# Kernel optimization log

Measured on AMD Instinct MI355X. Metric: run time of the kernel, lower is better.

Reference implementation:

```python
import jax, jax.numpy as jnp
import numpy as np

N, E, G = 200000, 1200000, 2048
NODE_DIM, H = 5, 64
NEG_SLOPE = 0.2


def setup_inputs() -> dict:
    key = jax.random.key(0)
    ks = jax.random.split(key, 20)
    def glorot(k, shape):
        fan = sum(shape) if len(shape) > 1 else shape[0] + 1
        return jax.random.normal(k, shape, jnp.float32) * jnp.sqrt(2.0 / fan)
    inp = {
        'x': jax.random.normal(ks[0], (N, NODE_DIM), jnp.float32),
        'edge_index': jax.random.randint(ks[1], (2, E), 0, N, jnp.int64),
        'batch': jnp.sort(jax.random.randint(ks[2], (N,), 0, G, jnp.int64)),
        'embed_W': glorot(ks[3], (NODE_DIM, H)), 'embed_b': jnp.zeros((H,), jnp.float32),
        'g1_W': glorot(ks[4], (H, H)), 'g1_asrc': glorot(ks[5], (H,)), 'g1_adst': glorot(ks[6], (H,)), 'g1_b': jnp.zeros((H,), jnp.float32),
        'g2_W': glorot(ks[7], (H, H)), 'g2_asrc': glorot(ks[8], (H,)), 'g2_adst': glorot(ks[9], (H,)), 'g2_b': jnp.zeros((H,), jnp.float32),
        'fc1_W': glorot(ks[10], (2 * H, 64)), 'fc1_b': jnp.zeros((64,), jnp.float32),
        'fc2_W': glorot(ks[11], (64, 32)), 'fc2_b': jnp.zeros((32,), jnp.float32),
        'fc3_W': glorot(ks[12], (32, 1)), 'fc3_b': jnp.zeros((1,), jnp.float32),
    }
    return inp


def gat_conv(x, src, dst, W, a_src, a_dst, b):
    # x: [N, H] -> h: [N, H]; edges (with self-loops) src->dst
    h = x @ W
    alpha_s = h @ a_src  # [N]
    alpha_d = h @ a_dst  # [N]
    e = jax.nn.leaky_relu(alpha_s[src] + alpha_d[dst], NEG_SLOPE)  # [E']
    m = jax.ops.segment_max(e, dst, num_segments=N)
    w = jnp.exp(e - m[dst])
    denom = jax.ops.segment_sum(w, dst, num_segments=N)
    alpha = w / (denom[dst] + 1e-16)
    out = jax.ops.segment_sum(h[src] * alpha[:, None], dst, num_segments=N)
    return out + b


def reference(x, edge_index, batch, embed_W, embed_b,
              g1_W, g1_asrc, g1_adst, g1_b,
              g2_W, g2_asrc, g2_adst, g2_b,
              fc1_W, fc1_b, fc2_W, fc2_b, fc3_W, fc3_b):
    # add self loops once (PyG GATConv default add_self_loops=True)
    loops = jnp.arange(N, dtype=edge_index.dtype)
    src = jnp.concatenate([edge_index[0], loops])
    dst = jnp.concatenate([edge_index[1], loops])

    h = x @ embed_W + embed_b
    h = gat_conv(h, src, dst, g1_W, g1_asrc, g1_adst, g1_b)
    h = jax.nn.relu(h)
    h = gat_conv(h, src, dst, g2_W, g2_asrc, g2_adst, g2_b)

    # global mean / max pooling per graph
    cnt = jax.ops.segment_sum(jnp.ones((N,), h.dtype), batch, num_segments=G)
    mean = jax.ops.segment_sum(h, batch, num_segments=G) / jnp.maximum(cnt, 1.0)[:, None]
    mx = jax.ops.segment_max(h, batch, num_segments=G)
    mx = jnp.where(cnt[:, None] > 0, mx, 0.0)
    g = jnp.concatenate([mean, mx], axis=1)  # [G, 2H]

    g = jax.nn.relu(g @ fc1_W + fc1_b)
    g = jax.nn.relu(g @ fc2_W + fc2_b)
    return g @ fc3_W + fc3_b  # [G, 1]
```

## Files before the change

### kernel.cpp

```cpp
#include <hip/hip_runtime.h>
#include <hip/hip_bf16.h>
#include <hip/hip_fp16.h>

#define HD 64
#define NODE_DIM 5
#define NEG_SLOPE 0.2f
#define GT 64
#define BSH 9
#define BNODES 512
#define NBMAX 512
#define BCAP 4096
#define EPB 8
#define LDH 72

typedef _Float16 f16x8 __attribute__((ext_vector_type(8)));
typedef float f32x4 __attribute__((ext_vector_type(4)));

template <bool EMBED>
__global__ __launch_bounds__(256) void gemm_alpha_k(
    const void* __restrict__ hin, const float* __restrict__ embW,
    const float* __restrict__ embB, const float* __restrict__ W,
    const float* __restrict__ asrc, const float* __restrict__ adst,
    __half* __restrict__ hout, float* __restrict__ alpha_s,
    float* __restrict__ alpha_d, int* __restrict__ bcnt0, int N) {
    __shared__ _Float16 hs[GT * LDH];
    __shared__ _Float16 Wt[HD * LDH];
    __shared__ float xe[GT * NODE_DIM];
    __shared__ float we[NODE_DIM * HD + HD];
    const int t = threadIdx.x;
    const int n0 = blockIdx.x * GT;
    if (EMBED && blockIdx.x == 0) {
        for (int j = t; j < NBMAX; j += 256) bcnt0[j] = 0;
    }
    if (n0 >= N) return;
    const int rem = N - n0;

#pragma unroll
    for (int j = 0; j < 16; j++) {
        int idx = t + 256 * j;
        int k = idx >> 6, n = idx & 63;
        Wt[n * LDH + k] = (_Float16)W[idx];
    }

    if (EMBED) {
        const float* xin = (const float*)hin;
        for (int j = t; j < GT * NODE_DIM; j += 256)
            xe[j] = (j < rem * NODE_DIM) ? xin[(size_t)n0 * NODE_DIM + j] : 0.0f;
        for (int j = t; j < NODE_DIM * HD + HD; j += 256)
            we[j] = (j < NODE_DIM * HD) ? embW[j] : embB[j - NODE_DIM * HD];
        __syncthreads();
        int r = t >> 2, d0 = (t & 3) * 16;
#pragma unroll
        for (int jj = 0; jj < 16; jj++) {
            int d = d0 + jj;
            float acc = we[NODE_DIM * HD + d];
#pragma unroll
            for (int k = 0; k < NODE_DIM; k++)
                acc = fmaf(xe[r * NODE_DIM + k], we[k * HD + d], acc);
            hs[r * LDH + d] = (r < rem) ? (_Float16)acc : (_Float16)0.0f;
        }
    } else {
        const short4* g4 = (const short4*)((const __half*)hin + (size_t)n0 * HD);
#pragma unroll
        for (int j = 0; j < 4; j++) {
            int idx = t + 256 * j;
            int row = idx >> 4, c4 = idx & 15;
            short4 v = {0, 0, 0, 0};
            if (row < rem) v = g4[idx];
            *(short4*)(hs + row * LDH + c4 * 4) = v;
        }
    }
    __syncthreads();

    const int lane = t & 63;
    const int w = t >> 6;
    const int r16 = lane & 15;
    const int g = lane >> 4;

    const _Float16* hrow = hs + (w * 16 + r16) * LDH + g * 8;
    f16x8 b0 = *(const f16x8*)(hrow);
    f16x8 b1 = *(const f16x8*)(hrow + 32);

    f32x4 acc[4];
#pragma unroll
    for (int mt = 0; mt < 4; mt++) acc[mt] = (f32x4){0.f, 0.f, 0.f, 0.f};

#pragma unroll
    for (int mt = 0; mt < 4; mt++) {
        const _Float16* arow = Wt + (mt * 16 + r16) * LDH + g * 8;
        f16x8 a0 = *(const f16x8*)(arow);
        f16x8 a1 = *(const f16x8*)(arow + 32);
        acc[mt] = __builtin_amdgcn_mfma_f32_16x16x32_f16(a0, b0, acc[mt], 0, 0, 0);
        acc[mt] = __builtin_amdgcn_mfma_f32_16x16x32_f16(a1, b1, acc[mt], 0, 0, 0);
    }

    const int node = n0 + w * 16 + r16;
    float ps = 0.0f, pd = 0.0f;
    if (node < N) {
#pragma unroll
        for (int mt = 0; mt < 4; mt++) {
            float4 av = ((const float4*)asrc)[mt * 4 + g];
            float4 bv = ((const float4*)adst)[mt * 4 + g];
            ps += acc[mt][0] * av.x + acc[mt][1] * av.y +
                  acc[mt][2] * av.z + acc[mt][3] * av.w;
            pd += acc[mt][0] * bv.x + acc[mt][1] * bv.y +
                  acc[mt][2] * bv.z + acc[mt][3] * bv.w;
            short4 s;
            s.x = __half_as_short(__float2half_rn(acc[mt][0]));
            s.y = __half_as_short(__float2half_rn(acc[mt][1]));
            s.z = __half_as_short(__float2half_rn(acc[mt][2]));
            s.w = __half_as_short(__float2half_rn(acc[mt][3]));
            ((short4*)hout)[(size_t)node * 16 + mt * 4 + g] = s;
        }
    }
    ps += __shfl_xor(ps, 16);
    ps += __shfl_xor(ps, 32);
    pd += __shfl_xor(pd, 16);
    pd += __shfl_xor(pd, 32);
    if (g == 0 && node < N) {
        alpha_s[node] = ps;
        alpha_d[node] = pd;
    }
}


__global__ __launch_bounds__(256) void partition_k(
    const int* __restrict__ ei, int* __restrict__ bcnt,
    int* __restrict__ bpack, int E) {
    __shared__ int lcnt[NBMAX], lbase[NBMAX];
    int dst[EPB], src[EPB];
    int jb = blockIdx.x * (256 * EPB) + threadIdx.x;
#pragma unroll
    for (int u = 0; u < EPB; u++) {
        int j = jb + u * 256;
        if (j < E) {
            dst[u] = __builtin_nontemporal_load(&ei[E + j]);
            src[u] = __builtin_nontemporal_load(&ei[j]);
        } else dst[u] = -1;
    }
    for (int b = threadIdx.x; b < NBMAX; b += 256) lcnt[b] = 0;
    __syncthreads();
#pragma unroll
    for (int u = 0; u < EPB; u++)
        if (dst[u] >= 0) atomicAdd(&lcnt[dst[u] >> BSH], 1);
    __syncthreads();
    for (int b = threadIdx.x; b < NBMAX; b += 256) {
        int c = lcnt[b];
        lbase[b] = c ? (b * BCAP + atomicAdd(&bcnt[b], c)) : 0;
        lcnt[b] = 0;
    }
    __syncthreads();
#pragma unroll
    for (int u = 0; u < EPB; u++) {
        if (dst[u] >= 0) {
            int b = dst[u] >> BSH;
            int o = atomicAdd(&lcnt[b], 1);
            bpack[lbase[b] + o] = (src[u] << BSH) | (dst[u] & (BNODES - 1));
        }
    }
}

__global__ __launch_bounds__(256) void bucket_csr_k(
    const int* __restrict__ bpack, const int* __restrict__ bcnt,
    int* __restrict__ off, int* __restrict__ csr_src, int N, int NB) {
    __shared__ int s[BNODES];
    __shared__ int lcur[BNODES];
    __shared__ int sred[256];
    const int t = threadIdx.x;
    const int b = blockIdx.x;
    const int nbase = b << BSH;
    const int cnt = bcnt[b];
    const int w0 = b * BCAP;

    int part = 0;
    for (int j = t; j < b; j += 256) part += bcnt[j];
    sred[t] = part;
    s[t] = 0; s[t + 256] = 0;
    __syncthreads();
#pragma unroll
    for (int o = 128; o; o >>= 1) {
        if (t < o) sred[t] += sred[t + o];
        __syncthreads();
    }
    const int e0 = sred[0];

    for (int j = t; j < cnt; j += 256)
        atomicAdd(&s[bpack[w0 + j] & (BNODES - 1)], 1);
    __syncthreads();
    int d0 = s[t], d1 = s[t + 256];
#pragma unroll
    for (int o = 1; o < BNODES; o <<= 1) {
        int a0 = (t >= o) ? s[t - o] : 0;
        int a1 = (t + 256 >= o) ? s[t + 256 - o] : 0;
        __syncthreads();
        s[t] += a0;
        s[t + 256] += a1;
        __syncthreads();
    }
    int ex0 = s[t] - d0, ex1 = s[t + 256] - d1;
    lcur[t] = ex0; lcur[t + 256] = ex1;
    int n0 = nbase + t, n1 = nbase + t + 256;
    if (n0 < N) off[n0] = e0 + ex0;
    if (n1 < N) off[n1] = e0 + ex1;
    if (t == 0 && b == NB - 1) off[N] = e0 + cnt;
    __syncthreads();
    for (int j = t; j < cnt; j += 256) {
        int v = bpack[w0 + j];
        int pos = atomicAdd(&lcur[v & (BNODES - 1)], 1);
        csr_src[e0 + pos] = v >> BSH;
    }
}

template <bool BR>
__global__ __launch_bounds__(256) void gather_k(
    const int* __restrict__ off, const int* __restrict__ csr_src,
    const float* __restrict__ as, const float* __restrict__ ad,
    const __half* __restrict__ h, const float* __restrict__ bias,
    __half* __restrict__ out, int N) {
    int tid = blockIdx.x * blockDim.x + threadIdx.x;
    int wv = tid >> 6;
    int lane = threadIdx.x & 63;
    int grp = lane >> 4;
    int l16 = lane & 15;
    int n = wv * 4 + grp;
    if (n >= N) return;
    int s0 = off[n], s1 = off[n + 1];
    float adv = ad[n];
    const short4* h4 = (const short4*)h;

    float e = as[n] + adv;
    e = (e >= 0.0f) ? e : NEG_SLOPE * e;
    float wsl = __expf(e);
    float l0 = wsl, l1 = 0.0f;
    short4 hvs = h4[(unsigned)(n * 16 + l16)];
    float4 acc0, acc1 = {0, 0, 0, 0};
    acc0.x = wsl * __half2float(__short_as_half(hvs.x));
    acc0.y = wsl * __half2float(__short_as_half(hvs.y));
    acc0.z = wsl * __half2float(__short_as_half(hvs.z));
    acc0.w = wsl * __half2float(__short_as_half(hvs.w));

    const int last = s1 - 1;
    for (int i = s0; i < s1; i += 8) {
        int src[8];
        short4 hv[8];
        float wt[8];
#pragma unroll
        for (int u = 0; u < 8; u++) {
            int idx = i + u;
            src[u] = csr_src[idx < s1 ? idx : last];
        }
#pragma unroll
        for (int u = 0; u < 8; u++)
            hv[u] = h4[(unsigned)(src[u] * 16 + l16)];
#pragma unroll
        for (int u = 0; u < 8; u++) {
            float e0 = as[src[u]] + adv;
            e0 = (e0 >= 0.0f) ? e0 : NEG_SLOPE * e0;
            float w0 = __expf(e0);
            wt[u] = (i + u < s1) ? w0 : 0.0f;
        }
#pragma unroll
        for (int u = 0; u < 8; u += 2) {
            l0 += wt[u];
            l1 += wt[u + 1];
            acc0.x = fmaf(wt[u], __half2float(__short_as_half(hv[u].x)), acc0.x);
            acc0.y = fmaf(wt[u], __half2float(__short_as_half(hv[u].y)), acc0.y);
            acc0.z = fmaf(wt[u], __half2float(__short_as_half(hv[u].z)), acc0.z);
            acc0.w = fmaf(wt[u], __half2float(__short_as_half(hv[u].w)), acc0.w);
            acc1.x = fmaf(wt[u + 1], __half2float(__short_as_half(hv[u + 1].x)), acc1.x);
            acc1.y = fmaf(wt[u + 1], __half2float(__short_as_half(hv[u + 1].y)), acc1.y);
            acc1.z = fmaf(wt[u + 1], __half2float(__short_as_half(hv[u + 1].z)), acc1.z);
            acc1.w = fmaf(wt[u + 1], __half2float(__short_as_half(hv[u + 1].w)), acc1.w);
        }
    }
    float inv = 1.0f / (l0 + l1 + 1e-16f);
    float4 r;
    r.x = (acc0.x + acc1.x) * inv;
    r.y = (acc0.y + acc1.y) * inv;
    r.z = (acc0.z + acc1.z) * inv;
    r.w = (acc0.w + acc1.w) * inv;
    if (BR) {
        float4 b = ((const float4*)bias)[l16];
        r.x = fmaxf(r.x + b.x, 0.0f);
        r.y = fmaxf(r.y + b.y, 0.0f);
        r.z = fmaxf(r.z + b.z, 0.0f);
        r.w = fmaxf(r.w + b.w, 0.0f);
    }
    short4 o;
    o.x = __half_as_short(__float2half_rn(r.x));
    o.y = __half_as_short(__float2half_rn(r.y));
    o.z = __half_as_short(__float2half_rn(r.z));
    o.w = __half_as_short(__float2half_rn(r.w));
    ((short4*)out)[(unsigned)(n * 16 + l16)] = o;
}

__global__ __launch_bounds__(256) void pool_mlp_k(
    const __half* __restrict__ hfin, const float* __restrict__ hb,
    const int* __restrict__ batch, int N,
    const float* __restrict__ fc1W, const float* __restrict__ fc1b,
    const float* __restrict__ fc2W, const float* __restrict__ fc2b,
    const float* __restrict__ fc3W, const float* __restrict__ fc3b,
    float* __restrict__ out) {
    __shared__ float psum[16][64];
    __shared__ float pmax[16][64];
    __shared__ float lds[192];
    int g = blockIdx.x;
    int t = threadIdx.x;
    int gg = t >> 4;
    int l16 = t & 15;
    int lo = 0, hi = N;
    while (lo < hi) { int mid = (lo + hi) >> 1; if (batch[mid] < g) lo = mid + 1; else hi = mid; }
    int start = lo;
    lo = start; hi = N;
    while (lo < hi) { int mid = (lo + hi) >> 1; if (batch[mid] < g + 1) lo = mid + 1; else hi = mid; }
    int end = lo;
    const short4* h4 = (const short4*)hfin;
    float4 sum = {0, 0, 0, 0};
    float4 mx = {-INFINITY, -INFINITY, -INFINITY, -INFINITY};
    for (int n = start + gg; n < end; n += 16) {
        short4 v = h4[(size_t)n * 16 + l16];
        float a = __half2float(__short_as_half(v.x));
        float b = __half2float(__short_as_half(v.y));
        float c = __half2float(__short_as_half(v.z));
        float d = __half2float(__short_as_half(v.w));
        sum.x += a; sum.y += b; sum.z += c; sum.w += d;
        mx.x = fmaxf(mx.x, a); mx.y = fmaxf(mx.y, b);
        mx.z = fmaxf(mx.z, c); mx.w = fmaxf(mx.w, d);
    }
    *(float4*)&psum[gg][l16 * 4] = sum;
    *(float4*)&pmax[gg][l16 * 4] = mx;
    __syncthreads();
    if (t < 64) {
        float s = 0.0f, m = -INFINITY;
#pragma unroll
        for (int k = 0; k < 16; k++) {
            s += psum[k][t];
            m = fmaxf(m, pmax[k][t]);
        }
        int cnt = end - start;
        float bias = hb[t];
        lds[t]      = (cnt > 0) ? s / (float)cnt + bias : 0.0f;
        lds[64 + t] = (cnt > 0) ? m + bias : 0.0f;
    }
    __syncthreads();
    if (t < 64) {
        int lane = t;
        float o1 = fc1b[lane];
        for (int k = 0; k < 128; k++) o1 += lds[k] * fc1W[k * 64 + lane];
        o1 = fmaxf(o1, 0.0f);
        __builtin_amdgcn_s_barrier();
        lds[128 + lane] = o1;
        float o2 = 0.0f;
        if (lane < 32) {
            o2 = fc2b[lane];
            for (int k = 0; k < 64; k++) o2 += lds[128 + k] * fc2W[k * 32 + lane];
            o2 = fmaxf(o2, 0.0f);
        }
        float part = (lane < 32) ? o2 * fc3W[lane] : 0.0f;
#pragma unroll
        for (int off = 32; off; off >>= 1) part += __shfl_xor(part, off);
        if (lane == 0) out[g] = part + fc3b[0];
    }
}

static inline size_t align256(size_t x) { return (x + 255) & ~(size_t)255; }

extern "C" void kernel_launch(void* const* d_in, const int* in_sizes, int n_in,
                              void* d_out, int out_size, void* d_ws, size_t ws_size,
                              hipStream_t stream) {
    const float* x      = (const float*)d_in[0];
    const int*   ei     = (const int*)d_in[1];
    const int*   batch  = (const int*)d_in[2];
    const float* embW   = (const float*)d_in[3];
    const float* embB   = (const float*)d_in[4];
    const float* g1W    = (const float*)d_in[5];
    const float* g1as   = (const float*)d_in[6];
    const float* g1ad   = (const float*)d_in[7];
    const float* g1b    = (const float*)d_in[8];
    const float* g2W    = (const float*)d_in[9];
    const float* g2as   = (const float*)d_in[10];
    const float* g2ad   = (const float*)d_in[11];
    const float* g2b    = (const float*)d_in[12];
    const float* fc1W   = (const float*)d_in[13];
    const float* fc1b   = (const float*)d_in[14];
    const float* fc2W   = (const float*)d_in[15];
    const float* fc2b   = (const float*)d_in[16];
    const float* fc3W   = (const float*)d_in[17];
    const float* fc3b   = (const float*)d_in[18];
    float* out = (float*)d_out;

    const int N  = in_sizes[0] / NODE_DIM;
    const int E  = in_sizes[1] / 2;
    const int G  = out_size;
    const int NH = N * HD;
    const int NB = (N + BNODES - 1) >> BSH;

    char* ws = (char*)d_ws;
    __half* bufA    = (__half*)ws; ws += align256((size_t)NH * 2);
    __half* bufB    = (__half*)ws; ws += align256((size_t)NH * 2);
    float*  as_buf  = (float*)ws;  ws += align256((size_t)N * 4);
    float*  ad_buf  = (float*)ws;  ws += align256((size_t)N * 4);
    int*    off     = (int*)ws;    ws += align256((size_t)(N + 1) * 4);
    int*    bcnt    = (int*)ws;    ws += align256((size_t)NBMAX * 4);
    int*    bpack   = (int*)ws;    ws += align256((size_t)NB * BCAP * 4);
    int*    csrsrc  = (int*)ws;    ws += align256((size_t)E * 4);

    const int B = 256;
    dim3 blk(B);
    dim3 gr_gemm((N + GT - 1) / GT);
    dim3 gr_gath(((N + 3) / 4 * 64 + B - 1) / B);
    dim3 gr_epb((E + B * EPB - 1) / (B * EPB));

    gemm_alpha_k<true><<<gr_gemm, blk, 0, stream>>>(x, embW, embB, g1W, g1as, g1ad,
                                                    bufB, as_buf, ad_buf, bcnt, N);
    partition_k<<<gr_epb, blk, 0, stream>>>(ei, bcnt, bpack, E);
    bucket_csr_k<<<dim3(NB), blk, 0, stream>>>(bpack, bcnt, off, csrsrc, N, NB);

    gather_k<true><<<gr_gath, blk, 0, stream>>>(off, csrsrc, as_buf, ad_buf,
                                                bufB, g1b, bufA, N);

    gemm_alpha_k<false><<<gr_gemm, blk, 0, stream>>>(bufA, nullptr, nullptr, g2W,
                                                     g2as, g2ad, bufB, as_buf, ad_buf,
                                                     nullptr, N);
    gather_k<false><<<gr_gath, blk, 0, stream>>>(off, csrsrc, as_buf, ad_buf,
                                                 bufB, nullptr, bufA, N);

    pool_mlp_k<<<dim3(G), dim3(256), 0, stream>>>(bufA, g2b, batch, N,
                                                  fc1W, fc1b, fc2W, fc2b, fc3W, fc3b, out);
}
```

Baseline: 262.5 us.

## Fuse embedding GEMM and edge partition into one interleaved launch, sort partition writes

Merges the layer-1 embed+GEMM kernel and the edge partition kernel into a single launch whose blocks are interleaved by role, so the two independent stages can run concurrently on the GPU. The partition blocks now sort edges in shared memory by bucket with a prefix scan before writing, so the bpack stores go out in contiguous runs instead of scattered. The bucket counters are zeroed by a separate tiny kernel, which adds one launch. It also adds a shared-memory scan with many barriers and a per-element binary search.

```diff
diff --git a/kernel.cpp b/kernel.cpp
--- a/kernel.cpp
+++ b/kernel.cpp
@@ -16,22 +16,108 @@
 typedef _Float16 f16x8 __attribute__((ext_vector_type(8)));
 typedef float f32x4 __attribute__((ext_vector_type(4)));
 
-template <bool EMBED>
-__global__ __launch_bounds__(256) void gemm_alpha_k(
-    const void* __restrict__ hin, const float* __restrict__ embW,
+
+__global__ void zero_k(int* __restrict__ p, int total) {
+    int i = blockIdx.x * blockDim.x + threadIdx.x;
+    if (i < total) p[i] = 0;
+}
+
+union FusedSM {
+    struct {
+        _Float16 hs[GT * LDH];
+        _Float16 Wt[HD * LDH];
+        float xe[GT * NODE_DIM];
+        float we[NODE_DIM * HD + HD];
+    } g;
+    struct {
+        int lcnt[NBMAX];
+        int lbase[NBMAX];
+        int lexc[NBMAX];
+        int cur[NBMAX];
+        int sorted[256 * EPB];
+    } p;
+};
+
+__global__ __launch_bounds__(256) void fused_embed_part_k(
+    const float* __restrict__ xin, const float* __restrict__ embW,
     const float* __restrict__ embB, const float* __restrict__ W,
     const float* __restrict__ asrc, const float* __restrict__ adst,
     __half* __restrict__ hout, float* __restrict__ alpha_s,
-    float* __restrict__ alpha_d, int* __restrict__ bcnt0, int N) {
-    __shared__ _Float16 hs[GT * LDH];
-    __shared__ _Float16 Wt[HD * LDH];
-    __shared__ float xe[GT * NODE_DIM];
-    __shared__ float we[NODE_DIM * HD + HD];
+    float* __restrict__ alpha_d, int N,
+    const int* __restrict__ ei, int* __restrict__ bcnt,
+    int* __restrict__ bpack, int E, int PB, int TOT) {
+    __shared__ FusedSM sm;
     const int t = threadIdx.x;
-    const int n0 = blockIdx.x * GT;
-    if (EMBED && blockIdx.x == 0) {
-        for (int j = t; j < NBMAX; j += 256) bcnt0[j] = 0;
-    }
+    const int bid = blockIdx.x;
+    const int p_before = (int)(((long long)bid * PB) / TOT);
+    const int p_after  = (int)(((long long)(bid + 1) * PB) / TOT);
+    const bool is_part = p_after > p_before;
+
+    if (is_part) {
+        const int pbid = p_before;
+        int dst[EPB], src[EPB];
+        int jb = pbid * (256 * EPB) + t;
+#pragma unroll
+        for (int u = 0; u < EPB; u++) {
+            int j = jb + u * 256;
+            if (j < E) {
+                dst[u] = __builtin_nontemporal_load(&ei[E + j]);
+                src[u] = __builtin_nontemporal_load(&ei[j]);
+            } else dst[u] = -1;
+        }
+        sm.p.lcnt[t] = 0; sm.p.lcnt[t + 256] = 0;
+        __syncthreads();
+#pragma unroll
+        for (int u = 0; u < EPB; u++)
+            if (dst[u] >= 0) atomicAdd(&sm.p.lcnt[dst[u] >> BSH], 1);
+        __syncthreads();
+        sm.p.lexc[t] = sm.p.lcnt[t];
+        sm.p.lexc[t + 256] = sm.p.lcnt[t + 256];
+        __syncthreads();
+        int c0 = sm.p.lexc[t], c1 = sm.p.lexc[t + 256];
+#pragma unroll
+        for (int o = 1; o < NBMAX; o <<= 1) {
+            int a0 = (t >= o) ? sm.p.lexc[t - o] : 0;
+            int a1 = (t + 256 >= o) ? sm.p.lexc[t + 256 - o] : 0;
+            __syncthreads();
+            sm.p.lexc[t] += a0;
+            sm.p.lexc[t + 256] += a1;
+            __syncthreads();
+        }
+        int e0 = sm.p.lexc[t] - c0, e1 = sm.p.lexc[t + 256] - c1;
+        __syncthreads();
+        sm.p.lexc[t] = e0; sm.p.lexc[t + 256] = e1;
+        sm.p.cur[t] = e0;  sm.p.cur[t + 256] = e1;
+        {
+            int c = sm.p.lcnt[t];
+            sm.p.lbase[t] = c ? t * BCAP + atomicAdd(&bcnt[t], c) : 0;
+            c = sm.p.lcnt[t + 256];
+            sm.p.lbase[t + 256] = c ? (t + 256) * BCAP + atomicAdd(&bcnt[t + 256], c) : 0;
+        }
+        __syncthreads();
+#pragma unroll
+        for (int u = 0; u < EPB; u++) {
+            if (dst[u] >= 0) {
+                int b = dst[u] >> BSH;
+                int pp = atomicAdd(&sm.p.cur[b], 1);
+                sm.p.sorted[pp] = (src[u] << BSH) | (dst[u] & (BNODES - 1));
+            }
+        }
+        __syncthreads();
+        const int tot = sm.p.lexc[NBMAX - 1] + sm.p.lcnt[NBMAX - 1];
+        for (int j = t; j < tot; j += 256) {
+            int lo = 0, hi = NBMAX - 1;
+            while (lo < hi) {
+                int mid = (lo + hi + 1) >> 1;
+                if (sm.p.lexc[mid] <= j) lo = mid; else hi = mid - 1;
+            }
+            bpack[sm.p.lbase[lo] + (j - sm.p.lexc[lo])] = sm.p.sorted[j];
+        }
+        return;
+    }
+
+    const int gidx = bid - p_before;
+    const int n0 = gidx * GT;
     if (n0 >= N) return;
     const int rem = N - n0;
 
@@ -39,35 +125,23 @@
     for (int j = 0; j < 16; j++) {
         int idx = t + 256 * j;
         int k = idx >> 6, n = idx & 63;
-        Wt[n * LDH + k] = (_Float16)W[idx];
-    }
-
-    if (EMBED) {
-        const float* xin = (const float*)hin;
-        for (int j = t; j < GT * NODE_DIM; j += 256)
-            xe[j] = (j < rem * NODE_DIM) ? xin[(size_t)n0 * NODE_DIM + j] : 0.0f;
-        for (int j = t; j < NODE_DIM * HD + HD; j += 256)
-            we[j] = (j < NODE_DIM * HD) ? embW[j] : embB[j - NODE_DIM * HD];
-        __syncthreads();
+        sm.g.Wt[n * LDH + k] = (_Float16)W[idx];
+    }
+    for (int j = t; j < GT * NODE_DIM; j += 256)
+        sm.g.xe[j] = (j < rem * NODE_DIM) ? xin[(size_t)n0 * NODE_DIM + j] : 0.0f;
+    for (int j = t; j < NODE_DIM * HD + HD; j += 256)
+        sm.g.we[j] = (j < NODE_DIM * HD) ? embW[j] : embB[j - NODE_DIM * HD];
+    __syncthreads();
+    {
         int r = t >> 2, d0 = (t & 3) * 16;
 #pragma unroll
         for (int jj = 0; jj < 16; jj++) {
             int d = d0 + jj;
-            float acc = we[NODE_DIM * HD + d];
+            float acc = sm.g.we[NODE_DIM * HD + d];
 #pragma unroll
             for (int k = 0; k < NODE_DIM; k++)
-                acc = fmaf(xe[r * NODE_DIM + k], we[k * HD + d], acc);
-            hs[r * LDH + d] = (r < rem) ? (_Float16)acc : (_Float16)0.0f;
-        }
-    } else {
-        const short4* g4 = (const short4*)((const __half*)hin + (size_t)n0 * HD);
-#pragma unroll
-        for (int j = 0; j < 4; j++) {
-            int idx = t + 256 * j;
-            int row = idx >> 4, c4 = idx & 15;
-            short4 v = {0, 0, 0, 0};
-            if (row < rem) v = g4[idx];
-            *(short4*)(hs + row * LDH + c4 * 4) = v;
+                acc = fmaf(sm.g.xe[r * NODE_DIM + k], sm.g.we[k * HD + d], acc);
+            sm.g.hs[r * LDH + d] = (r < rem) ? (_Float16)acc : (_Float16)0.0f;
         }
     }
     __syncthreads();
@@ -77,17 +151,16 @@
     const int r16 = lane & 15;
     const int g = lane >> 4;
 
-    const _Float16* hrow = hs + (w * 16 + r16) * LDH + g * 8;
+    const _Float16* hrow = sm.g.hs + (w * 16 + r16) * LDH + g * 8;
     f16x8 b0 = *(const f16x8*)(hrow);
     f16x8 b1 = *(const f16x8*)(hrow + 32);
 
     f32x4 acc[4];
 #pragma unroll
     for (int mt = 0; mt < 4; mt++) acc[mt] = (f32x4){0.f, 0.f, 0.f, 0.f};
-
 #pragma unroll
     for (int mt = 0; mt < 4; mt++) {
-        const _Float16* arow = Wt + (mt * 16 + r16) * LDH + g * 8;
+        const _Float16* arow = sm.g.Wt + (mt * 16 + r16) * LDH + g * 8;
         f16x8 a0 = *(const f16x8*)(arow);
         f16x8 a1 = *(const f16x8*)(arow + 32);
         acc[mt] = __builtin_amdgcn_mfma_f32_16x16x32_f16(a0, b0, acc[mt], 0, 0, 0);
@@ -123,40 +196,84 @@
     }
 }
 
-
-__global__ __launch_bounds__(256) void partition_k(
-    const int* __restrict__ ei, int* __restrict__ bcnt,
-    int* __restrict__ bpack, int E) {
-    __shared__ int lcnt[NBMAX], lbase[NBMAX];
-    int dst[EPB], src[EPB];
-    int jb = blockIdx.x * (256 * EPB) + threadIdx.x;
-#pragma unroll
-    for (int u = 0; u < EPB; u++) {
-        int j = jb + u * 256;
-        if (j < E) {
-            dst[u] = __builtin_nontemporal_load(&ei[E + j]);
-            src[u] = __builtin_nontemporal_load(&ei[j]);
-        } else dst[u] = -1;
-    }
-    for (int b = threadIdx.x; b < NBMAX; b += 256) lcnt[b] = 0;
-    __syncthreads();
-#pragma unroll
-    for (int u = 0; u < EPB; u++)
-        if (dst[u] >= 0) atomicAdd(&lcnt[dst[u] >> BSH], 1);
-    __syncthreads();
-    for (int b = threadIdx.x; b < NBMAX; b += 256) {
-        int c = lcnt[b];
-        lbase[b] = c ? (b * BCAP + atomicAdd(&bcnt[b], c)) : 0;
-        lcnt[b] = 0;
-    }
-    __syncthreads();
-#pragma unroll
-    for (int u = 0; u < EPB; u++) {
-        if (dst[u] >= 0) {
-            int b = dst[u] >> BSH;
-            int o = atomicAdd(&lcnt[b], 1);
-            bpack[lbase[b] + o] = (src[u] << BSH) | (dst[u] & (BNODES - 1));
-        }
+__global__ __launch_bounds__(256) void gemm_alpha_k(
+    const __half* __restrict__ hin, const float* __restrict__ W,
+    const float* __restrict__ asrc, const float* __restrict__ adst,
+    __half* __restrict__ hout, float* __restrict__ alpha_s,
+    float* __restrict__ alpha_d, int N) {
+    __shared__ _Float16 hs[GT * LDH];
+    __shared__ _Float16 Wt[HD * LDH];
+    const int t = threadIdx.x;
+    const int n0 = blockIdx.x * GT;
+    if (n0 >= N) return;
+    const int rem = N - n0;
+
+#pragma unroll
+    for (int j = 0; j < 16; j++) {
+        int idx = t + 256 * j;
+        int k = idx >> 6, n = idx & 63;
+        Wt[n * LDH + k] = (_Float16)W[idx];
+    }
+    {
+        const short4* g4 = (const short4*)(hin + (size_t)n0 * HD);
+#pragma unroll
+        for (int j = 0; j < 4; j++) {
+            int idx = t + 256 * j;
+            int row = idx >> 4, c4 = idx & 15;
+            short4 v = {0, 0, 0, 0};
+            if (row < rem) v = g4[idx];
+            *(short4*)(hs + row * LDH + c4 * 4) = v;
+        }
+    }
+    __syncthreads();
+
+    const int lane = t & 63;
+    const int w = t >> 6;
+    const int r16 = lane & 15;
+    const int g = lane >> 4;
+
+    const _Float16* hrow = hs + (w * 16 + r16) * LDH + g * 8;
+    f16x8 b0 = *(const f16x8*)(hrow);
+    f16x8 b1 = *(const f16x8*)(hrow + 32);
+
+    f32x4 acc[4];
+#pragma unroll
+    for (int mt = 0; mt < 4; mt++) acc[mt] = (f32x4){0.f, 0.f, 0.f, 0.f};
+#pragma unroll
+    for (int mt = 0; mt < 4; mt++) {
+        const _Float16* arow = Wt + (mt * 16 + r16) * LDH + g * 8;
+        f16x8 a0 = *(const f16x8*)(arow);
+        f16x8 a1 = *(const f16x8*)(arow + 32);
+        acc[mt] = __builtin_amdgcn_mfma_f32_16x16x32_f16(a0, b0, acc[mt], 0, 0, 0);
+        acc[mt] = __builtin_amdgcn_mfma_f32_16x16x32_f16(a1, b1, acc[mt], 0, 0, 0);
+    }
+
+    const int node = n0 + w * 16 + r16;
+    float ps = 0.0f, pd = 0.0f;
+    if (node < N) {
+#pragma unroll
+        for (int mt = 0; mt < 4; mt++) {
+            float4 av = ((const float4*)asrc)[mt * 4 + g];
+            float4 bv = ((const float4*)adst)[mt * 4 + g];
+            ps += acc[mt][0] * av.x + acc[mt][1] * av.y +
+                  acc[mt][2] * av.z + acc[mt][3] * av.w;
+            pd += acc[mt][0] * bv.x + acc[mt][1] * bv.y +
+                  acc[mt][2] * bv.z + acc[mt][3] * bv.w;
+            short4 s;
+            s.x = __half_as_short(__float2half_rn(acc[mt][0]));
+            s.y = __half_as_short(__float2half_rn(acc[mt][1]));
+            s.z = __half_as_short(__float2half_rn(acc[mt][2]));
+            s.w = __half_as_short(__float2half_rn(acc[mt][3]));
+            ((short4*)hout)[(size_t)node * 16 + mt * 4 + g] = s;
+        }
+    }
+    ps += __shfl_xor(ps, 16);
+    ps += __shfl_xor(ps, 32);
+    pd += __shfl_xor(pd, 16);
+    pd += __shfl_xor(pd, 32);
+    if (g == 0 && node < N) {
+        alpha_s[node] = ps;
+        alpha_d[node] = pd;
     }
 }
 
@@ -407,21 +524,22 @@
 
     const int B = 256;
     dim3 blk(B);
-    dim3 gr_gemm((N + GT - 1) / GT);
+    const int GB = (N + GT - 1) / GT;
+    const int PB = (E + B * EPB - 1) / (B * EPB);
+    const int TOT = GB + PB;
     dim3 gr_gath(((N + 3) / 4 * 64 + B - 1) / B);
-    dim3 gr_epb((E + B * EPB - 1) / (B * EPB));
-
-    gemm_alpha_k<true><<<gr_gemm, blk, 0, stream>>>(x, embW, embB, g1W, g1as, g1ad,
-                                                    bufB, as_buf, ad_buf, bcnt, N);
-    partition_k<<<gr_epb, blk, 0, stream>>>(ei, bcnt, bpack, E);
+
+    zero_k<<<dim3(2), blk, 0, stream>>>(bcnt, NBMAX);
+    fused_embed_part_k<<<dim3(TOT), blk, 0, stream>>>(
+        x, embW, embB, g1W, g1as, g1ad, bufB, as_buf, ad_buf, N,
+        ei, bcnt, bpack, E, PB, TOT);
     bucket_csr_k<<<dim3(NB), blk, 0, stream>>>(bpack, bcnt, off, csrsrc, N, NB);
 
     gather_k<true><<<gr_gath, blk, 0, stream>>>(off, csrsrc, as_buf, ad_buf,
                                                 bufB, g1b, bufA, N);
 
-    gemm_alpha_k<false><<<gr_gemm, blk, 0, stream>>>(bufA, nullptr, nullptr, g2W,
-                                                     g2as, g2ad, bufB, as_buf, ad_buf,
-                                                     nullptr, N);
+    gemm_alpha_k<<<dim3(GB), blk, 0, stream>>>(bufA, g2W, g2as, g2ad,
+                                               bufB, as_buf, ad_buf, N);
     gather_k<false><<<gr_gath, blk, 0, stream>>>(off, csrsrc, as_buf, ad_buf,
                                                  bufB, nullptr, bufA, N);
 
```

New measurement: 256.5 us. 1.02x faster.
